# Optimization experiments

Measured on AMD Instinct MI355X. Metric: run time of the kernel, lower is better.

## Reference

```python
import jax, jax.numpy as jnp
import numpy as np

B, S, D = 1, 4096, 1024
H, Dh = 16, 64
F = 4096  # mlp_factor * D
EPS = 1e-6


def _ln(x, scale, bias=None):
    m = jnp.mean(x, axis=-1, keepdims=True)
    v = jnp.var(x, axis=-1, keepdims=True)
    y = (x - m) * jax.lax.rsqrt(v + EPS) * scale
    return y + bias if bias is not None else y


def setup_inputs() -> dict:
    key = jax.random.key(0)
    ks = jax.random.split(key, 10)
    lecun = lambda k, shape, fan_in: (jax.random.normal(k, shape, jnp.float32) * (fan_in ** -0.5))
    inp = {
        "x": jax.random.normal(ks[0], (B, S, D), jnp.float32),
        # causal mask, broadcastable to [B, H, S, S]
        "mask": jnp.tril(jnp.ones((S, S), bool))[None, None],
        # PreNorm (TPNorm -> LayerNorm)
        "ln_scale": jnp.ones((D,), jnp.float32),
        "ln_bias": jnp.zeros((D,), jnp.float32),
        # MLP input projection
        "w_in": lecun(ks[1], (D, F), D),
        "b_in": jnp.zeros((F,), jnp.float32),
        # QKV projection
        "wq": lecun(ks[2], (D, H, Dh), D),
        "bq": jnp.zeros((H, Dh), jnp.float32),
        "wk": lecun(ks[3], (D, H, Dh), D),
        "bk": jnp.zeros((H, Dh), jnp.float32),
        "wv": lecun(ks[4], (D, H, Dh), D),
        "bv": jnp.zeros((H, Dh), jnp.float32),
        # qk-norm scales (normalize_qk=True)
        "qn_scale": jnp.ones((Dh,), jnp.float32),
        "kn_scale": jnp.ones((Dh,), jnp.float32),
        # MLP output projection
        "w_mo": lecun(ks[5], (F, D), F),
        "b_mo": jnp.zeros((D,), jnp.float32),
        # Attention output projection
        "w_ao": lecun(ks[6], (H * Dh, D), H * Dh),
        "b_ao": jnp.zeros((D,), jnp.float32),
    }
    return inp


def reference(x, mask, ln_scale, ln_bias, w_in, b_in, wq, bq, wk, bk, wv, bv,
              qn_scale, kn_scale, w_mo, b_mo, w_ao, b_ao):
    residual = x
    xn = _ln(x, ln_scale, ln_bias)

    # fused QKV + MLP-input projections (QKVMLPDenseParallel)
    h = jax.nn.gelu(jnp.einsum("bsd,df->bsf", xn, w_in) + b_in)  # [B,S,F]
    q = jnp.einsum("bsd,dhk->bshk", xn, wq) + bq  # [B,S,H,Dh]
    k = jnp.einsum("bsd,dhk->bshk", xn, wk) + bk
    v = jnp.einsum("bsd,dhk->bshk", xn, wv) + bv
    # normalize_qk: per-head LayerNorm (no bias) on q, k
    q = _ln(q, qn_scale)
    k = _ln(k, kn_scale)

    # dot-product attention
    scores = jnp.einsum("bqhd,bkhd->bhqk", q, k) / np.sqrt(Dh).astype(np.float32)
    scores = jnp.where(mask, scores, jnp.finfo(scores.dtype).min)
    attn = jax.nn.softmax(scores, axis=-1)
    o = jnp.einsum("bhqk,bkhd->bqhd", attn, v)  # [B,S,H,Dh]

    # fused attention-out + MLP-out projections (AttnMLPOutParallel)
    mlp_out = jnp.einsum("bsf,fd->bsd", h, w_mo) + b_mo
    attn_out = jnp.einsum("bse,ed->bsd", o.reshape(B, S, H * Dh), w_ao) + b_ao

    # dropout deterministic (train=False); residual add
    return residual + mlp_out + attn_out
```

## Files before the change

### kernel.cpp

```cpp
#include <hip/hip_runtime.h>
#include <hip/hip_fp16.h>

typedef _Float16 half8 __attribute__((ext_vector_type(8)));
typedef float floatx4 __attribute__((ext_vector_type(4)));

constexpr int kS = 4096;
constexpr int kD = 1024;
constexpr int kH = 16;
constexpr int kDh = 64;
constexpr int kF = 4096;
constexpr int kNQKV = kF + 3 * kD;
constexpr int kKOut = kF + kD;

__device__ __forceinline__ void async_ld16(const void* g, void* l) {
  __builtin_amdgcn_global_load_lds(
      (const __attribute__((address_space(1))) void*)g,
      (__attribute__((address_space(3))) void*)l, 16, 0, 0);
}

__global__ __launch_bounds__(256) void wtrans_all(
    const float* __restrict__ w_in, const float* __restrict__ wq,
    const float* __restrict__ wk, const float* __restrict__ wv,
    const float* __restrict__ w_mo, const float* __restrict__ w_ao,
    _Float16* __restrict__ Wqkv, _Float16* __restrict__ Wout) {
  __shared__ float t[32][33];
  int id = blockIdx.x;
  const float* src; _Float16* dst; int N, ldk, noff, koff, nt, kt;
  if (id < 4096)       { src = w_in; dst = Wqkv; N = kF; ldk = kD; noff = 0;        koff = 0;  nt = id & 127; kt = id >> 7; }
  else if (id < 5120)  { id -= 4096; src = wq;  dst = Wqkv; N = kD; ldk = kD; noff = kF;       koff = 0;  nt = id & 31; kt = id >> 5; }
  else if (id < 6144)  { id -= 5120; src = wk;  dst = Wqkv; N = kD; ldk = kD; noff = kF + kD;  koff = 0;  nt = id & 31; kt = id >> 5; }
  else if (id < 7168)  { id -= 6144; src = wv;  dst = Wqkv; N = kD; ldk = kD; noff = kF + 2*kD; koff = 0; nt = id & 31; kt = id >> 5; }
  else if (id < 11264) { id -= 7168; src = w_mo; dst = Wout; N = kD; ldk = kKOut; noff = 0;    koff = 0;  nt = id & 31; kt = id >> 5; }
  else                 { id -= 11264; src = w_ao; dst = Wout; N = kD; ldk = kKOut; noff = 0;   koff = kF; nt = id & 31; kt = id >> 5; }
  const int tid = threadIdx.x;
  const int n0 = nt * 32, k0 = kt * 32;
#pragma unroll
  for (int i = 0; i < 4; ++i) {
    const int kl = (tid >> 5) + i * 8, nl = tid & 31;
    t[kl][nl] = src[(size_t)(k0 + kl) * N + n0 + nl];
  }
  __syncthreads();
#pragma unroll
  for (int i = 0; i < 4; ++i) {
    const int nl = (tid >> 5) + i * 8, kl = tid & 31;
    dst[(size_t)(noff + n0 + nl) * ldk + koff + k0 + kl] = (_Float16)t[kl][nl];
  }
}

__global__ __launch_bounds__(256) void htrans_kernel(
    const _Float16* __restrict__ src, _Float16* __restrict__ dst, int R, int C) {
  __shared__ _Float16 t[32][34];
  const int tid = threadIdx.x;
  const int c0 = blockIdx.x * 32, r0 = blockIdx.y * 32;
#pragma unroll
  for (int i = 0; i < 4; ++i) {
    const int rl = (tid >> 5) + i * 8, cl = tid & 31;
    t[rl][cl] = src[(size_t)(r0 + rl) * C + c0 + cl];
  }
  __syncthreads();
#pragma unroll
  for (int i = 0; i < 4; ++i) {
    const int cl = (tid >> 5) + i * 8, rl = tid & 31;
    dst[(size_t)(c0 + cl) * R + r0 + rl] = t[rl][cl];
  }
}

__global__ __launch_bounds__(256) void biasprep_kernel(
    const float* b_in, const float* bq, const float* bk, const float* bv,
    const float* b_mo, const float* b_ao, float* bcat, float* bsum) {
  const int i = blockIdx.x * 256 + threadIdx.x;
  if (i < kF) bcat[i] = b_in[i];
  else if (i < kF + kD) bcat[i] = bq[i - kF];
  else if (i < kF + 2 * kD) bcat[i] = bk[i - kF - kD];
  else if (i < kNQKV) bcat[i] = bv[i - kF - 2 * kD];
  else if (i < kNQKV + kD) bsum[i - kNQKV] = b_mo[i - kNQKV] + b_ao[i - kNQKV];
}

__global__ __launch_bounds__(256) void ln_kernel(
    const float* __restrict__ x, const float* __restrict__ scale,
    const float* __restrict__ bias, _Float16* __restrict__ xn) {
  const int row = blockIdx.x;
  const int tid = threadIdx.x;
  const float* xr = x + (size_t)row * kD;
  float v[4];
  float s = 0.f, sq = 0.f;
#pragma unroll
  for (int i = 0; i < 4; ++i) {
    v[i] = xr[tid + 256 * i];
    s += v[i];
    sq += v[i] * v[i];
  }
  for (int off = 32; off; off >>= 1) {
    s += __shfl_xor(s, off);
    sq += __shfl_xor(sq, off);
  }
  __shared__ float red[8];
  const int wv = tid >> 6;
  if ((tid & 63) == 0) { red[wv] = s; red[wv + 4] = sq; }
  __syncthreads();
  s = red[0] + red[1] + red[2] + red[3];
  sq = red[4] + red[5] + red[6] + red[7];
  const float mean = s * (1.0f / kD);
  const float var = sq * (1.0f / kD) - mean * mean;
  const float rstd = rsqrtf(var + 1e-6f);
#pragma unroll
  for (int i = 0; i < 4; ++i) {
    int d = tid + 256 * i;
    xn[(size_t)row * kD + d] = (_Float16)((v[i] - mean) * rstd * scale[d] + bias[d]);
  }
}

__device__ __forceinline__ float fast_gelu(float xv) {
  const float z = 0.7978845608028654f * (xv + 0.044715f * xv * xv * xv);
  const float u = exp2f(fminf(2.885390081777927f * z, 80.0f));
  return xv * u / (1.0f + u);
}

__global__ __launch_bounds__(256) void gemm_qkvin(
    const _Float16* __restrict__ A, const _Float16* __restrict__ Bp,
    const float* __restrict__ bcat, const float* __restrict__ qn_scale,
    const float* __restrict__ kn_scale, _Float16* __restrict__ ho,
    _Float16* __restrict__ q, _Float16* __restrict__ k, _Float16* __restrict__ v) {
  __shared__ alignas(16) _Float16 Ts[16 * 512];
  _Float16* As = Ts;
  _Float16* Bs = Ts + 8 * 512;

  const int tid = threadIdx.x;
  const int lane = tid & 63;
  const int wave = tid >> 6;
  const int wm = (wave >> 1) * 64;
  const int wn = (wave & 1) * 64;
  const int m0 = blockIdx.x * 128;
  const int n0 = blockIdx.y * 128;
  const int lrow = lane & 15;
  const int quad = lane >> 4;

  floatx4 acc[4][4] = {};

  for (int k0 = 0; k0 < kD; k0 += 32) {
    __syncthreads();
#pragma unroll
    for (int i = 0; i < 4; ++i) {
      const int chunk = wave * 4 + i;
      const int r = ((chunk & 7) << 4) + (lane >> 2);
      const int csrc = ((lane & 3) ^ ((r >> 1) & 3)) << 3;
      const _Float16* src = (chunk < 8)
          ? A + (size_t)(m0 + r) * kD + k0 + csrc
          : Bp + (size_t)(n0 + r) * kD + k0 + csrc;
      async_ld16(src, Ts + chunk * 512);
    }
    __syncthreads();

    half8 af[4], bf[4];
#pragma unroll
    for (int i = 0; i < 4; ++i) {
      const int ra = wm + i * 16 + lrow;
      const int rb = wn + i * 16 + lrow;
      af[i] = *reinterpret_cast<const half8*>(&As[ra * 32 + ((quad ^ ((ra >> 1) & 3)) << 3)]);
      bf[i] = *reinterpret_cast<const half8*>(&Bs[rb * 32 + ((quad ^ ((rb >> 1) & 3)) << 3)]);
    }
#pragma unroll
    for (int i = 0; i < 4; ++i)
#pragma unroll
      for (int j = 0; j < 4; ++j)
        acc[i][j] = __builtin_amdgcn_mfma_f32_16x16x32_f16(af[i], bf[j], acc[i][j], 0, 0, 0);
  }

  const int nblk = n0 + wn;
  if (nblk < kF) {
#pragma unroll
    for (int i = 0; i < 4; ++i) {
      const int gm = m0 + wm + i * 16 + quad * 4;
#pragma unroll
      for (int j = 0; j < 4; ++j) {
        const int gn = nblk + j * 16 + lrow;
        const float bn = bcat[gn];
#pragma unroll
        for (int r = 0; r < 4; ++r)
          ho[(size_t)(gm + r) * kKOut + gn] = (_Float16)fast_gelu(acc[i][j][r] + bn);
      }
    }
  } else if (nblk >= kF + 2 * kD) {
#pragma unroll
    for (int i = 0; i < 4; ++i) {
      const int gm = m0 + wm + i * 16 + quad * 4;
#pragma unroll
      for (int j = 0; j < 4; ++j) {
        const int gn = nblk + j * 16 + lrow;
        const float bn = bcat[gn];
#pragma unroll
        for (int r = 0; r < 4; ++r)
          v[(size_t)(gm + r) * kD + ((gn - kF) & (kD - 1))] = (_Float16)(acc[i][j][r] + bn);
      }
    }
  } else {
    const bool isq = nblk < kF + kD;
    const float* nsc = isq ? qn_scale : kn_scale;
    const float sm = isq ? 0.18033688f : 1.0f;
    _Float16* dst = isq ? q : k;
    const int col0 = (nblk - kF) & (kD - 1);
    float bj[4];
#pragma unroll
    for (int j = 0; j < 4; ++j) bj[j] = bcat[nblk + j * 16 + lrow];
#pragma unroll
    for (int i = 0; i < 4; ++i) {
      const int gm = m0 + wm + i * 16 + quad * 4;
#pragma unroll
      for (int r = 0; r < 4; ++r) {
        float vals[4], s1 = 0.f, s2 = 0.f;
#pragma unroll
        for (int j = 0; j < 4; ++j) {
          const float vv = acc[i][j][r] + bj[j];
          vals[j] = vv; s1 += vv; s2 += vv * vv;
        }
#pragma unroll
        for (int off = 1; off <= 8; off <<= 1) {
          s1 += __shfl_xor(s1, off);
          s2 += __shfl_xor(s2, off);
        }
        const float mean = s1 * (1.0f / 64.0f);
        const float rstd = rsqrtf(s2 * (1.0f / 64.0f) - mean * mean + 1e-6f);
#pragma unroll
        for (int j = 0; j < 4; ++j) {
          const int d = j * 16 + lrow;
          dst[(size_t)(gm + r) * kD + col0 + d] =
              (_Float16)((vals[j] - mean) * rstd * nsc[d] * sm);
        }
      }
    }
  }
}

__global__ __launch_bounds__(256) void initout_kernel(
    const float* __restrict__ x, const float* __restrict__ bsum,
    float* __restrict__ out) {
  const int i = blockIdx.x * 256 + threadIdx.x;
  out[i] = x[i] + bsum[i & (kD - 1)];
}

__global__ __launch_bounds__(256) void gemm_out(
    const _Float16* __restrict__ A, const _Float16* __restrict__ Bp,
    float* __restrict__ out) {
  __shared__ alignas(16) _Float16 Ts[16 * 512];
  _Float16* As = Ts;
  _Float16* Bs = Ts + 8 * 512;

  const int tid = threadIdx.x;
  const int lane = tid & 63;
  const int wave = tid >> 6;
  const int wm = (wave >> 1) * 64;
  const int wn = (wave & 1) * 64;
  const int m0 = blockIdx.x * 128;
  const int n0 = blockIdx.y * 128;
  const int kbeg = blockIdx.z * (kKOut / 2);
  const int lrow = lane & 15;
  const int quad = lane >> 4;

  floatx4 acc[4][4] = {};

  for (int k0 = kbeg; k0 < kbeg + kKOut / 2; k0 += 32) {
    __syncthreads();
#pragma unroll
    for (int i = 0; i < 4; ++i) {
      const int chunk = wave * 4 + i;
      const int r = ((chunk & 7) << 4) + (lane >> 2);
      const int csrc = ((lane & 3) ^ ((r >> 1) & 3)) << 3;
      const _Float16* src = (chunk < 8)
          ? A + (size_t)(m0 + r) * kKOut + k0 + csrc
          : Bp + (size_t)(n0 + r) * kKOut + k0 + csrc;
      async_ld16(src, Ts + chunk * 512);
    }
    __syncthreads();

    half8 af[4], bf[4];
#pragma unroll
    for (int i = 0; i < 4; ++i) {
      const int ra = wm + i * 16 + lrow;
      const int rb = wn + i * 16 + lrow;
      af[i] = *reinterpret_cast<const half8*>(&As[ra * 32 + ((quad ^ ((ra >> 1) & 3)) << 3)]);
      bf[i] = *reinterpret_cast<const half8*>(&Bs[rb * 32 + ((quad ^ ((rb >> 1) & 3)) << 3)]);
    }
#pragma unroll
    for (int i = 0; i < 4; ++i)
#pragma unroll
      for (int j = 0; j < 4; ++j)
        acc[i][j] = __builtin_amdgcn_mfma_f32_16x16x32_f16(af[i], bf[j], acc[i][j], 0, 0, 0);
  }

#pragma unroll
  for (int i = 0; i < 4; ++i) {
    const int gm = m0 + wm + i * 16 + quad * 4;
#pragma unroll
    for (int j = 0; j < 4; ++j) {
      const int gn = n0 + wn + j * 16 + lrow;
#pragma unroll
      for (int r = 0; r < 4; ++r)
        atomicAdd(out + (size_t)(gm + r) * kD + gn, acc[i][j][r]);
    }
  }
}

__global__ __launch_bounds__(256) void zeroacc_kernel(float* __restrict__ p, int n) {
  const int i = blockIdx.x * 256 + threadIdx.x;
  if (i < n) p[i] = 0.f;
}

__global__ __launch_bounds__(256) void fattn_kernel(
    const _Float16* __restrict__ Q, const _Float16* __restrict__ K,
    const _Float16* __restrict__ Vt, float* __restrict__ Oacc,
    float* __restrict__ Lacc) {
  __shared__ alignas(16) _Float16 Qs[128 * 64];
  __shared__ alignas(16) _Float16 Ks[64 * 64];
  __shared__ alignas(16) _Float16 Vs[64 * 64];
  __shared__ alignas(16) _Float16 Ps[128 * 72];

  const int tid = threadIdx.x;
  const int lane = tid & 63;
  const int wave = tid >> 6;
  const int lrow = lane & 15;
  const int quad = lane >> 4;

  const int id = blockIdx.x;
  const int xcd = id & 7;
  const int idx = id >> 3;
  const int h = (xcd << 1) | (idx & 1);
  const int rem = idx >> 1;
  const int pair = rem & 15;
  const int split = rem >> 4;

  const int rs = lane >> 3;
  const int cs = lane & 7;
  constexpr float kOff = 11.5415603f;

  for (int pass = 0; pass < 2; ++pass) {
    const int qtile = pass ? (31 - pair) : pair;
    const int qbase = qtile * 128;

    __syncthreads();
#pragma unroll
    for (int i = 0; i < 4; ++i) {
      const int chunk = wave * 4 + i;
      const int r = chunk * 8 + rs;
      async_ld16(Q + (size_t)(qbase + r) * kD + h * kDh + ((cs ^ (r & 7)) << 3),
                 Qs + chunk * 512);
    }
    __syncthreads();

    half8 qf[2][2];
#pragma unroll
    for (int i = 0; i < 2; ++i)
#pragma unroll
      for (int kt = 0; kt < 2; ++kt) {
        const int row = wave * 32 + i * 16 + lrow;
        qf[i][kt] = *reinterpret_cast<const half8*>(
            &Qs[row * 64 + (((kt * 4 + quad) ^ (row & 7)) << 3)]);
      }

    float lst[2][4] = {};
    floatx4 oacc[2][4] = {};
    const int qw = qbase + wave * 32;
    const int tmax = 2 * qtile + 1;

    for (int t = split; t <= tmax; t += 3) {
      const int k0 = t * 64;
      __syncthreads();
#pragma unroll
      for (int i = 0; i < 4; ++i) {
        const int c2 = wave * 4 + i;
        if (c2 < 8) {
          const int r = c2 * 8 + rs;
          async_ld16(K + (size_t)(k0 + r) * kD + h * kDh + ((cs ^ (r & 7)) << 3),
                     Ks + c2 * 512);
        } else {
          const int c = c2 - 8;
          const int r = c * 8 + rs;
          async_ld16(Vt + (size_t)(h * kDh + r) * kS + k0 + ((cs ^ (r & 7)) << 3),
                     Vs + c * 512);
        }
      }
      __syncthreads();

      if (k0 > qw + 31) continue;

      const bool diag = (k0 + 63 > qw);
      floatx4 sacc[2][4] = {};
#pragma unroll
      for (int jt = 0; jt < 4; ++jt) {
        if (diag && (k0 + jt * 16 > qw + 31)) continue;
#pragma unroll
        for (int kt = 0; kt < 2; ++kt) {
          const int rb = jt * 16 + lrow;
          half8 bfk = *reinterpret_cast<const half8*>(
              &Ks[rb * 64 + (((kt * 4 + quad) ^ (rb & 7)) << 3)]);
          sacc[0][jt] = __builtin_amdgcn_mfma_f32_16x16x32_f16(qf[0][kt], bfk, sacc[0][jt], 0, 0, 0);
          sacc[1][jt] = __builtin_amdgcn_mfma_f32_16x16x32_f16(qf[1][kt], bfk, sacc[1][jt], 0, 0, 0);
        }
      }

      if (diag) {
#pragma unroll
        for (int i = 0; i < 2; ++i)
#pragma unroll
          for (int jt = 0; jt < 4; ++jt) {
            const int kg = k0 + jt * 16 + lrow;
#pragma unroll
            for (int r = 0; r < 4; ++r)
              if (kg > qw + i * 16 + quad * 4 + r) sacc[i][jt][r] = -1e30f;
          }
      }

#pragma unroll
      for (int i = 0; i < 2; ++i)
#pragma unroll
        for (int jt = 0; jt < 4; ++jt)
#pragma unroll
          for (int r = 0; r < 4; ++r) {
            const float p = exp2f(sacc[i][jt][r] - kOff);
            sacc[i][jt][r] = p;
            lst[i][r] += p;
          }

#pragma unroll
      for (int i = 0; i < 2; ++i)
#pragma unroll
        for (int jt = 0; jt < 4; ++jt)
#pragma unroll
          for (int r = 0; r < 4; ++r)
            Ps[(wave * 32 + i * 16 + quad * 4 + r) * 72 + jt * 16 + lrow] =
                (_Float16)sacc[i][jt][r];

      const int ktmax = (k0 >= qw) ? 1 : 2;
      for (int kt = 0; kt < ktmax; ++kt) {
        half8 pf[2];
#pragma unroll
        for (int i = 0; i < 2; ++i)
          pf[i] = *reinterpret_cast<const half8*>(
              &Ps[(wave * 32 + i * 16 + lrow) * 72 + (kt * 4 + quad) * 8]);
#pragma unroll
        for (int jt = 0; jt < 4; ++jt) {
          const int rb = jt * 16 + lrow;
          half8 vf = *reinterpret_cast<const half8*>(
              &Vs[rb * 64 + (((kt * 4 + quad) ^ (rb & 7)) << 3)]);
          oacc[0][jt] = __builtin_amdgcn_mfma_f32_16x16x32_f16(pf[0], vf, oacc[0][jt], 0, 0, 0);
          oacc[1][jt] = __builtin_amdgcn_mfma_f32_16x16x32_f16(pf[1], vf, oacc[1][jt], 0, 0, 0);
        }
      }
    }

#pragma unroll
    for (int i = 0; i < 2; ++i)
#pragma unroll
      for (int r = 0; r < 4; ++r)
#pragma unroll
        for (int off = 8; off; off >>= 1) lst[i][r] += __shfl_xor(lst[i][r], off);
#pragma unroll
    for (int i = 0; i < 2; ++i)
#pragma unroll
      for (int r = 0; r < 4; ++r) {
        const int qg = qw + i * 16 + quad * 4 + r;
        if (lrow == 0) atomicAdd(Lacc + qg * kH + h, lst[i][r]);
#pragma unroll
        for (int jt = 0; jt < 4; ++jt)
          atomicAdd(Oacc + ((size_t)qg * kH + h) * kDh + jt * 16 + lrow, oacc[i][jt][r]);
      }
  }
}

__global__ __launch_bounds__(256) void norm_kernel(
    const float* __restrict__ Oacc, const float* __restrict__ Lacc,
    _Float16* __restrict__ ho) {
  const int idx = blockIdx.x * 256 + threadIdx.x;
  const int q = idx >> 10, rem = idx & 1023;
  const float l = Lacc[(q << 4) + (rem >> 6)];
  ho[(size_t)q * kKOut + kF + rem] = (_Float16)(Oacc[idx] / l);
}

extern "C" void kernel_launch(void* const* d_in, const int* in_sizes, int n_in,
                              void* d_out, int out_size, void* d_ws, size_t ws_size,
                              hipStream_t stream) {
  const float* x        = (const float*)d_in[0];
  const float* ln_scale = (const float*)d_in[2];
  const float* ln_bias  = (const float*)d_in[3];
  const float* w_in     = (const float*)d_in[4];
  const float* b_in     = (const float*)d_in[5];
  const float* wq       = (const float*)d_in[6];
  const float* bq       = (const float*)d_in[7];
  const float* wk       = (const float*)d_in[8];
  const float* bk       = (const float*)d_in[9];
  const float* wv       = (const float*)d_in[10];
  const float* bv       = (const float*)d_in[11];
  const float* qn_scale = (const float*)d_in[12];
  const float* kn_scale = (const float*)d_in[13];
  const float* w_mo     = (const float*)d_in[14];
  const float* b_mo     = (const float*)d_in[15];
  const float* w_ao     = (const float*)d_in[16];
  const float* b_ao     = (const float*)d_in[17];
  float* out = (float*)d_out;

  char* ws = (char*)d_ws;
  size_t off = 0;
  auto alloc = [&](size_t bytes) { char* p = ws + off; off += bytes; return p; };
  char* zone = (char*)alloc((size_t)kS * kD * 2 + (size_t)kNQKV * kD * 2);
  _Float16* xn   = (_Float16*)zone;
  _Float16* Wqkv = (_Float16*)(zone + (size_t)kS * kD * 2);
  float* Oacc = (float*)zone;
  float* Lacc = (float*)(zone + (size_t)kS * kD * 4);
  _Float16* Wout = (_Float16*)alloc((size_t)kD * kKOut * 2);
  float*    bcat = (float*)alloc((size_t)kNQKV * 4);
  float*    bsum = (float*)alloc((size_t)kD * 4);
  _Float16* ho   = (_Float16*)alloc((size_t)kS * kKOut * 2);
  _Float16* q_h  = (_Float16*)alloc((size_t)kS * kD * 2);
  _Float16* k_h  = (_Float16*)alloc((size_t)kS * kD * 2);
  _Float16* v_h  = (_Float16*)alloc((size_t)kS * kD * 2);
  _Float16* v_t  = (_Float16*)alloc((size_t)kS * kD * 2);

  wtrans_all<<<12288, 256, 0, stream>>>(w_in, wq, wk, wv, w_mo, w_ao, Wqkv, Wout);
  biasprep_kernel<<<(kNQKV + kD + 255) / 256, 256, 0, stream>>>(
      b_in, bq, bk, bv, b_mo, b_ao, bcat, bsum);
  ln_kernel<<<kS, 256, 0, stream>>>(x, ln_scale, ln_bias, xn);

  gemm_qkvin<<<dim3(kS / 128, kNQKV / 128), 256, 0, stream>>>(
      xn, Wqkv, bcat, qn_scale, kn_scale, ho, q_h, k_h, v_h);

  htrans_kernel<<<dim3(kD / 32, kS / 32), 256, 0, stream>>>(v_h, v_t, kS, kD);

  zeroacc_kernel<<<(kS * kD + kS * kH + 255) / 256, 256, 0, stream>>>(
      Oacc, kS * kD + kS * kH);

  fattn_kernel<<<768, 256, 0, stream>>>(q_h, k_h, v_t, Oacc, Lacc);

  norm_kernel<<<kS * kD / 256, 256, 0, stream>>>(Oacc, Lacc, ho);

  initout_kernel<<<kS * kD / 256, 256, 0, stream>>>(x, bsum, out);
  gemm_out<<<dim3(kS / 128, kD / 128, 2), 256, 0, stream>>>(ho, Wout, out);
}
```

Baseline: 494.1 us.

## Shrink attention query tile to 64 rows, split KV in two, fuse init kernels

The flash-attention kernel now uses 64-row query tiles, with each wave owning 16 rows instead of 32, and the KV range split two ways instead of three. Grid size goes from 768 to 1024 blocks, and per-block LDS and register use drop. The intent is better load balance and occupancy, and less wasted work on the causal diagonal, where waves skip masked key sub-tiles. Separately, the zero-accumulator kernel and the output-init kernel are merged into one launch. The cost is half the MFMA work per K/V load, i.e. less reuse of each loaded K/V tile.

```diff
diff --git a/kernel.cpp b/kernel.cpp
--- a/kernel.cpp
+++ b/kernel.cpp
@@ -231,11 +231,16 @@
   }
 }
 
-__global__ __launch_bounds__(256) void initout_kernel(
+__global__ __launch_bounds__(256) void prep_kernel(
     const float* __restrict__ x, const float* __restrict__ bsum,
-    float* __restrict__ out) {
+    float* __restrict__ out, float* __restrict__ Oacc, float* __restrict__ Lacc) {
   const int i = blockIdx.x * 256 + threadIdx.x;
-  out[i] = x[i] + bsum[i & (kD - 1)];
+  if (i < kS * kD) {
+    out[i] = x[i] + bsum[i & (kD - 1)];
+    Oacc[i] = 0.f;
+  } else if (i < kS * kD + kS * kH) {
+    Lacc[i - kS * kD] = 0.f;
+  }
 }
 
 __global__ __launch_bounds__(256) void gemm_out(
@@ -300,19 +305,14 @@
   }
 }
 
-__global__ __launch_bounds__(256) void zeroacc_kernel(float* __restrict__ p, int n) {
-  const int i = blockIdx.x * 256 + threadIdx.x;
-  if (i < n) p[i] = 0.f;
-}
-
 __global__ __launch_bounds__(256) void fattn_kernel(
     const _Float16* __restrict__ Q, const _Float16* __restrict__ K,
     const _Float16* __restrict__ Vt, float* __restrict__ Oacc,
     float* __restrict__ Lacc) {
-  __shared__ alignas(16) _Float16 Qs[128 * 64];
+  __shared__ alignas(16) _Float16 Qs[64 * 64];
   __shared__ alignas(16) _Float16 Ks[64 * 64];
   __shared__ alignas(16) _Float16 Vs[64 * 64];
-  __shared__ alignas(16) _Float16 Ps[128 * 72];
+  __shared__ alignas(16) _Float16 Ps[64 * 72];
 
   const int tid = threadIdx.x;
   const int lane = tid & 63;
@@ -325,43 +325,40 @@
   const int idx = id >> 3;
   const int h = (xcd << 1) | (idx & 1);
   const int rem = idx >> 1;
-  const int pair = rem & 15;
-  const int split = rem >> 4;
+  const int pair = rem & 31;
+  const int split = rem >> 5;
 
   const int rs = lane >> 3;
   const int cs = lane & 7;
   constexpr float kOff = 11.5415603f;
 
   for (int pass = 0; pass < 2; ++pass) {
-    const int qtile = pass ? (31 - pair) : pair;
-    const int qbase = qtile * 128;
+    const int qtile = pass ? (63 - pair) : pair;
+    const int qbase = qtile * 64;
 
     __syncthreads();
 #pragma unroll
-    for (int i = 0; i < 4; ++i) {
-      const int chunk = wave * 4 + i;
+    for (int i = 0; i < 2; ++i) {
+      const int chunk = wave * 2 + i;
       const int r = chunk * 8 + rs;
       async_ld16(Q + (size_t)(qbase + r) * kD + h * kDh + ((cs ^ (r & 7)) << 3),
                  Qs + chunk * 512);
     }
     __syncthreads();
 
-    half8 qf[2][2];
-#pragma unroll
-    for (int i = 0; i < 2; ++i)
-#pragma unroll
-      for (int kt = 0; kt < 2; ++kt) {
-        const int row = wave * 32 + i * 16 + lrow;
-        qf[i][kt] = *reinterpret_cast<const half8*>(
-            &Qs[row * 64 + (((kt * 4 + quad) ^ (row & 7)) << 3)]);
-      }
-
-    float lst[2][4] = {};
-    floatx4 oacc[2][4] = {};
-    const int qw = qbase + wave * 32;
-    const int tmax = 2 * qtile + 1;
-
-    for (int t = split; t <= tmax; t += 3) {
+    half8 qf[2];
+#pragma unroll
+    for (int kt = 0; kt < 2; ++kt) {
+      const int row = wave * 16 + lrow;
+      qf[kt] = *reinterpret_cast<const half8*>(
+          &Qs[row * 64 + (((kt * 4 + quad) ^ (row & 7)) << 3)]);
+    }
+
+    float lst[4] = {0.f, 0.f, 0.f, 0.f};
+    floatx4 oacc[4] = {};
+    const int qw = qbase + wave * 16;
+
+    for (int t = split; t <= qtile; t += 2) {
       const int k0 = t * 64;
       __syncthreads();
 #pragma unroll
@@ -380,89 +377,72 @@
       }
       __syncthreads();
 
-      if (k0 > qw + 31) continue;
-
-      const bool diag = (k0 + 63 > qw);
-      floatx4 sacc[2][4] = {};
+      const bool diag = (t == qtile);
+
+      floatx4 sacc[4] = {};
 #pragma unroll
       for (int jt = 0; jt < 4; ++jt) {
-        if (diag && (k0 + jt * 16 > qw + 31)) continue;
+        if (diag && jt > wave) continue;
 #pragma unroll
         for (int kt = 0; kt < 2; ++kt) {
           const int rb = jt * 16 + lrow;
           half8 bfk = *reinterpret_cast<const half8*>(
               &Ks[rb * 64 + (((kt * 4 + quad) ^ (rb & 7)) << 3)]);
-          sacc[0][jt] = __builtin_amdgcn_mfma_f32_16x16x32_f16(qf[0][kt], bfk, sacc[0][jt], 0, 0, 0);
-          sacc[1][jt] = __builtin_amdgcn_mfma_f32_16x16x32_f16(qf[1][kt], bfk, sacc[1][jt], 0, 0, 0);
+          sacc[jt] = __builtin_amdgcn_mfma_f32_16x16x32_f16(qf[kt], bfk, sacc[jt], 0, 0, 0);
         }
       }
 
       if (diag) {
 #pragma unroll
-        for (int i = 0; i < 2; ++i)
-#pragma unroll
-          for (int jt = 0; jt < 4; ++jt) {
-            const int kg = k0 + jt * 16 + lrow;
-#pragma unroll
-            for (int r = 0; r < 4; ++r)
-              if (kg > qw + i * 16 + quad * 4 + r) sacc[i][jt][r] = -1e30f;
-          }
-      }
-
-#pragma unroll
-      for (int i = 0; i < 2; ++i)
-#pragma unroll
-        for (int jt = 0; jt < 4; ++jt)
-#pragma unroll
-          for (int r = 0; r < 4; ++r) {
-            const float p = exp2f(sacc[i][jt][r] - kOff);
-            sacc[i][jt][r] = p;
-            lst[i][r] += p;
-          }
-
-#pragma unroll
-      for (int i = 0; i < 2; ++i)
-#pragma unroll
-        for (int jt = 0; jt < 4; ++jt)
+        for (int jt = 0; jt < 4; ++jt) {
+          const int kg = k0 + jt * 16 + lrow;
 #pragma unroll
           for (int r = 0; r < 4; ++r)
-            Ps[(wave * 32 + i * 16 + quad * 4 + r) * 72 + jt * 16 + lrow] =
-                (_Float16)sacc[i][jt][r];
-
-      const int ktmax = (k0 >= qw) ? 1 : 2;
+            if (kg > qw + quad * 4 + r) sacc[jt][r] = -1e30f;
+        }
+      }
+
+#pragma unroll
+      for (int jt = 0; jt < 4; ++jt)
+#pragma unroll
+        for (int r = 0; r < 4; ++r) {
+          const float p = exp2f(sacc[jt][r] - kOff);
+          sacc[jt][r] = p;
+          lst[r] += p;
+        }
+
+#pragma unroll
+      for (int jt = 0; jt < 4; ++jt)
+#pragma unroll
+        for (int r = 0; r < 4; ++r)
+          Ps[(wave * 16 + quad * 4 + r) * 72 + jt * 16 + lrow] = (_Float16)sacc[jt][r];
+
+      const int ktmax = (diag && wave < 2) ? 1 : 2;
       for (int kt = 0; kt < ktmax; ++kt) {
-        half8 pf[2];
-#pragma unroll
-        for (int i = 0; i < 2; ++i)
-          pf[i] = *reinterpret_cast<const half8*>(
-              &Ps[(wave * 32 + i * 16 + lrow) * 72 + (kt * 4 + quad) * 8]);
+        half8 pf = *reinterpret_cast<const half8*>(
+            &Ps[(wave * 16 + lrow) * 72 + (kt * 4 + quad) * 8]);
 #pragma unroll
         for (int jt = 0; jt < 4; ++jt) {
           const int rb = jt * 16 + lrow;
           half8 vf = *reinterpret_cast<const half8*>(
               &Vs[rb * 64 + (((kt * 4 + quad) ^ (rb & 7)) << 3)]);
-          oacc[0][jt] = __builtin_amdgcn_mfma_f32_16x16x32_f16(pf[0], vf, oacc[0][jt], 0, 0, 0);
-          oacc[1][jt] = __builtin_amdgcn_mfma_f32_16x16x32_f16(pf[1], vf, oacc[1][jt], 0, 0, 0);
-        }
-      }
-    }
-
-#pragma unroll
-    for (int i = 0; i < 2; ++i)
-#pragma unroll
-      for (int r = 0; r < 4; ++r)
-#pragma unroll
-        for (int off = 8; off; off >>= 1) lst[i][r] += __shfl_xor(lst[i][r], off);
-#pragma unroll
-    for (int i = 0; i < 2; ++i)
-#pragma unroll
-      for (int r = 0; r < 4; ++r) {
-        const int qg = qw + i * 16 + quad * 4 + r;
-        if (lrow == 0) atomicAdd(Lacc + qg * kH + h, lst[i][r]);
-#pragma unroll
-        for (int jt = 0; jt < 4; ++jt)
-          atomicAdd(Oacc + ((size_t)qg * kH + h) * kDh + jt * 16 + lrow, oacc[i][jt][r]);
-      }
+          oacc[jt] = __builtin_amdgcn_mfma_f32_16x16x32_f16(pf, vf, oacc[jt], 0, 0, 0);
+        }
+      }
+    }
+
+#pragma unroll
+    for (int r = 0; r < 4; ++r)
+#pragma unroll
+      for (int off = 8; off; off >>= 1) lst[r] += __shfl_xor(lst[r], off);
+#pragma unroll
+    for (int r = 0; r < 4; ++r) {
+      const int qg = qw + quad * 4 + r;
+      if (lrow == 0) atomicAdd(Lacc + qg * kH + h, lst[r]);
+#pragma unroll
+      for (int jt = 0; jt < 4; ++jt)
+        atomicAdd(Oacc + ((size_t)qg * kH + h) * kDh + jt * 16 + lrow, oacc[jt][r]);
+    }
   }
 }
 
@@ -524,13 +504,12 @@
 
   htrans_kernel<<<dim3(kD / 32, kS / 32), 256, 0, stream>>>(v_h, v_t, kS, kD);
 
-  zeroacc_kernel<<<(kS * kD + kS * kH + 255) / 256, 256, 0, stream>>>(
-      Oacc, kS * kD + kS * kH);
-
-  fattn_kernel<<<768, 256, 0, stream>>>(q_h, k_h, v_t, Oacc, Lacc);
+  prep_kernel<<<(kS * kD + kS * kH + 255) / 256, 256, 0, stream>>>(
+      x, bsum, out, Oacc, Lacc);
+
+  fattn_kernel<<<1024, 256, 0, stream>>>(q_h, k_h, v_t, Oacc, Lacc);
 
   norm_kernel<<<kS * kD / 256, 256, 0, stream>>>(Oacc, Lacc, ho);
 
-  initout_kernel<<<kS * kD / 256, 256, 0, stream>>>(x, bsum, out);
   gemm_out<<<dim3(kS / 128, kD / 128, 2), 256, 0, stream>>>(ho, Wout, out);
 }
```

Measured after the change: 476.6 us. 3.5% less time.
